# Kernel optimization log

Hardware: AMD Instinct MI355X
Metric: run time of the kernel (lower is better)

## Reference

```python
import jax, jax.numpy as jnp
import numpy as np

TOP_K = 2

def _expert(x, w1, w2, w3):
    return (jax.nn.silu(x @ w1.T) * (x @ w3.T)) @ w2.T

def setup_inputs() -> dict:
    key = jax.random.key(0)
    ks = jax.random.split(key, 8)
    B, L, D, F, E, S = 4, 2048, 1024, 512, 16, 1
    p = lambda k, shape: (jax.random.normal(k, shape, jnp.float32) * 0.02)
    return {
        "x": jax.random.normal(ks[0], (B, L, D), jnp.float32),
        "gate_w": p(ks[1], (E, D)),
        "expert_bias": jnp.zeros((E,), jnp.float32),
        "sw1": p(ks[2], (S, F, D)),
        "sw2": p(ks[3], (S, D, F)),
        "sw3": p(ks[4], (S, F, D)),
        "ew1": p(ks[5], (E, F, D)),
        "ew2": p(ks[6], (E, D, F)),
        "ew3": p(ks[7], (E, F, D)),
    }

def reference(x, gate_w, expert_bias, sw1, sw2, sw3, ew1, ew2, ew3):
    B, L, D = x.shape
    E = gate_w.shape[0]
    flat_x = x.reshape(-1, D)  # [T, D], T = B*L

    # Shared experts (always-on)
    shared = sum(_expert(flat_x, sw1[i], sw2[i], sw3[i]) for i in range(sw1.shape[0]))

    # Router (eval mode: no jitter noise, no bias update; expert_bias buffer added)
    logits = flat_x @ gate_w.T + expert_bias          # [T, E]
    probs = jax.nn.softmax(logits, axis=-1)
    topw, topi = jax.lax.top_k(probs, TOP_K)          # [T, k]
    topw = topw / jnp.sum(topw, axis=-1, keepdims=True)

    # Routed experts: combine weight per (token, expert); zero weight => zero contribution,
    # identical math to the masked gather/scatter in the original.
    out = jnp.zeros_like(flat_x)
    for e in range(E):  # fixed small structural loop over experts
        cw = jnp.sum(jnp.where(topi == e, topw, 0.0), axis=-1)  # [T]
        out = out + cw[:, None] * _expert(flat_x, ew1[e], ew2[e], ew3[e])

    y = (shared + out).reshape(B, L, D)
    return y, probs
```

## Files before the change

### kernel.cpp

```cpp
#include <hip/hip_runtime.h>

typedef unsigned short u16;
typedef __bf16 bf16_t;
typedef bf16_t bf16x8 __attribute__((ext_vector_type(8)));
typedef float f32x4 __attribute__((ext_vector_type(4)));

#define T_TOK 8192
#define DIM   1024
#define FF    512
#define NE    16
#define RBASE_SHARED (2 * T_TOK)
#define NROWS (RBASE_SHARED + T_TOK)
#define MAXTILES 256
#define NSEG 512

__device__ __forceinline__ u16 f2bf(float f) {
  union { float f; unsigned u; } v; v.f = f;
  unsigned r = v.u + 0x7FFFu + ((v.u >> 16) & 1u);
  return (u16)(r >> 16);
}
__device__ __forceinline__ float bf2f(u16 h) {
  union { unsigned u; float f; } v; v.u = ((unsigned)h) << 16; return v.f;
}
__device__ __forceinline__ int clampi(int v, int lo, int hi) {
  return v < lo ? lo : (v > hi ? hi : v);
}

#define GLL16(g, l) __builtin_amdgcn_global_load_lds( \
    (const __attribute__((address_space(1))) void*)(g), \
    (__attribute__((address_space(3))) void*)(l), 16, 0, 0)

#define WAIT_VM_BARRIER(n) asm volatile("s_waitcnt vmcnt(" #n ")\n\ts_barrier" ::: "memory")
#define BARRIER_ONLY()     asm volatile("s_barrier" ::: "memory")
#define WAIT_LGKM0()       asm volatile("s_waitcnt lgkmcnt(0)" ::: "memory")

#define X4   2097152
#define SW4  131072
#define EW4  2097152
#define TOT4 (X4 + 3 * SW4 + 3 * EW4)

__global__ __launch_bounds__(256) void cvt_all_kernel(
    const float* __restrict__ x, const float* __restrict__ sw1,
    const float* __restrict__ sw2, const float* __restrict__ sw3,
    const float* __restrict__ ew1, const float* __restrict__ ew2,
    const float* __restrict__ ew3,
    u16* __restrict__ xb, u16* __restrict__ sw1b, u16* __restrict__ sw2b,
    u16* __restrict__ sw3b, u16* __restrict__ ew1b, u16* __restrict__ ew2b,
    u16* __restrict__ ew3b) {
  int i = blockIdx.x * 256 + threadIdx.x;
  const float* s; u16* dst; int j;
  if (i < X4)                       { s = x;   dst = xb;   j = i; }
  else if (i < X4 + SW4)            { s = sw1; dst = sw1b; j = i - X4; }
  else if (i < X4 + 2 * SW4)        { s = sw2; dst = sw2b; j = i - (X4 + SW4); }
  else if (i < X4 + 3 * SW4)        { s = sw3; dst = sw3b; j = i - (X4 + 2 * SW4); }
  else if (i < X4 + 3 * SW4 + EW4)      { s = ew1; dst = ew1b; j = i - (X4 + 3 * SW4); }
  else if (i < X4 + 3 * SW4 + 2 * EW4)  { s = ew2; dst = ew2b; j = i - (X4 + 3 * SW4 + EW4); }
  else if (i < TOT4)                    { s = ew3; dst = ew3b; j = i - (X4 + 3 * SW4 + 2 * EW4); }
  else return;
  float4 v = reinterpret_cast<const float4*>(s)[j];
  ushort4 o;
  o.x = f2bf(v.x); o.y = f2bf(v.y); o.z = f2bf(v.z); o.w = f2bf(v.w);
  reinterpret_cast<ushort4*>(dst)[j] = o;
}

__global__ __launch_bounds__(256) void router_kernel(
    const float* __restrict__ x, const float* __restrict__ gw,
    const float* __restrict__ ebias, float* __restrict__ probs,
    int* __restrict__ topi, float* __restrict__ topw, int* __restrict__ cnt_seg) {
  __shared__ int hist[16];
  int tid = threadIdx.x;
  int lane = tid & 63, w = tid >> 6;
  if (tid < 16) hist[tid] = 0;
  __syncthreads();
  const float4* gv = reinterpret_cast<const float4*>(gw);
  for (int it = 0; it < 2; ++it) {
    int t0 = blockIdx.x * 16 + (w + 4 * it) * 2;
    const float4* x0 = reinterpret_cast<const float4*>(x + (size_t)t0 * DIM);
    const float4* x1 = reinterpret_cast<const float4*>(x + (size_t)(t0 + 1) * DIM);
    float4 xa[4], xc[4];
#pragma unroll
    for (int j = 0; j < 4; ++j) { xa[j] = x0[j * 64 + lane]; xc[j] = x1[j * 64 + lane]; }
    float p0[16], p1[16];
#pragma unroll
    for (int e = 0; e < NE; ++e) {
      float s0 = 0.f, s1 = 0.f;
#pragma unroll
      for (int j = 0; j < 4; ++j) {
        float4 g = gv[e * 256 + j * 64 + lane];
        s0 += xa[j].x * g.x + xa[j].y * g.y + xa[j].z * g.z + xa[j].w * g.w;
        s1 += xc[j].x * g.x + xc[j].y * g.y + xc[j].z * g.z + xc[j].w * g.w;
      }
#pragma unroll
      for (int d = 1; d < 64; d <<= 1) { s0 += __shfl_xor(s0, d); s1 += __shfl_xor(s1, d); }
      float b = ebias[e];
      p0[e] = s0 + b; p1[e] = s1 + b;
    }
    float m0 = p0[0], m1 = p1[0];
#pragma unroll
    for (int e = 1; e < NE; ++e) { m0 = fmaxf(m0, p0[e]); m1 = fmaxf(m1, p1[e]); }
    float sum0 = 0.f, sum1 = 0.f;
#pragma unroll
    for (int e = 0; e < NE; ++e) {
      p0[e] = __expf(p0[e] - m0); sum0 += p0[e];
      p1[e] = __expf(p1[e] - m1); sum1 += p1[e];
    }
    float inv0 = 1.f / sum0, inv1 = 1.f / sum1;
#pragma unroll
    for (int e = 0; e < NE; ++e) { p0[e] *= inv0; p1[e] *= inv1; }
    if (lane == 0) {
#pragma unroll
      for (int j = 0; j < 4; ++j)
        reinterpret_cast<float4*>(probs + (size_t)t0 * NE)[j] =
            make_float4(p0[4 * j], p0[4 * j + 1], p0[4 * j + 2], p0[4 * j + 3]);
      float b1 = -1.f, b2 = -1.f; int i1 = 0, i2 = 0;
#pragma unroll
      for (int e = 0; e < NE; ++e) {
        float pe = p0[e];
        if (pe > b1) { b2 = b1; i2 = i1; b1 = pe; i1 = e; }
        else if (pe > b2) { b2 = pe; i2 = e; }
      }
      float ws = b1 + b2;
      reinterpret_cast<int2*>(topi)[t0] = make_int2(i1, i2);
      reinterpret_cast<float2*>(topw)[t0] = make_float2(b1 / ws, b2 / ws);
      atomicAdd(&hist[i1], 1); atomicAdd(&hist[i2], 1);
    }
    if (lane == 1) {
      int t1 = t0 + 1;
#pragma unroll
      for (int j = 0; j < 4; ++j)
        reinterpret_cast<float4*>(probs + (size_t)t1 * NE)[j] =
            make_float4(p1[4 * j], p1[4 * j + 1], p1[4 * j + 2], p1[4 * j + 3]);
      float b1 = -1.f, b2 = -1.f; int i1 = 0, i2 = 0;
#pragma unroll
      for (int e = 0; e < NE; ++e) {
        float pe = p1[e];
        if (pe > b1) { b2 = b1; i2 = i1; b1 = pe; i1 = e; }
        else if (pe > b2) { b2 = pe; i2 = e; }
      }
      float ws = b1 + b2;
      reinterpret_cast<int2*>(topi)[t1] = make_int2(i1, i2);
      reinterpret_cast<float2*>(topw)[t1] = make_float2(b1 / ws, b2 / ws);
      atomicAdd(&hist[i1], 1); atomicAdd(&hist[i2], 1);
    }
  }
  __syncthreads();
  if (tid < 16) cnt_seg[blockIdx.x * 16 + tid] = hist[tid];
}

__global__ __launch_bounds__(256) void scan_kernel(
    const int* __restrict__ cnt_seg, int* __restrict__ cnt, int* __restrict__ offs,
    int* __restrict__ seg_base, int2* __restrict__ tab) {
  __shared__ int chunk_sum[16][16];
  __shared__ int chunk_base[16][16];
  __shared__ int tot[16], off_s[17];
  int tid = threadIdx.x;
  int e = tid & 15, c = tid >> 4;
  int s0 = 0;
  for (int s = 0; s < 32; ++s) s0 += cnt_seg[(c * 32 + s) * 16 + e];
  chunk_sum[c][e] = s0;
  __syncthreads();
  if (tid < 16) {
    int r = 0;
    for (int c2 = 0; c2 < 16; ++c2) { chunk_base[c2][tid] = r; r += chunk_sum[c2][tid]; }
    tot[tid] = r;
  }
  __syncthreads();
  if (tid == 0) {
    int a = 0;
    for (int i = 0; i < 16; ++i) { off_s[i] = a; offs[i] = a; cnt[i] = tot[i]; a += tot[i]; }
    off_s[16] = RBASE_SHARED; offs[16] = RBASE_SHARED;
    for (int i = 0; i < MAXTILES; ++i) tab[i] = make_int2(-1, 0);
    int loadc[8]  = {0, 0, 0, 0, 0, 0, 0, 0};
    int cursor[8] = {0, 0, 0, 0, 0, 0, 0, 0};
    for (int g = 0; g < 16; ++g) {
      int nt = (tot[g] + 127) >> 7;
      if (nt == 0) continue;
      int best = 0;
      for (int c2 = 1; c2 < 8; ++c2) if (loadc[c2] < loadc[best]) best = c2;
      loadc[best] += nt;
      int c2 = best;
      for (int ti = 0; ti < nt; ++ti) {
        while (cursor[c2] >= 32) c2 = (c2 + 1) & 7;
        tab[c2 * 32 + cursor[c2]] = make_int2(g, ti * 128);
        cursor[c2]++;
      }
    }
    for (int ti = 0; ti < 64; ++ti) {
      int c2 = ti & 7;
      while (cursor[c2] >= 32) c2 = (c2 + 1) & 7;
      tab[c2 * 32 + cursor[c2]] = make_int2(16, ti * 128);
      cursor[c2]++;
    }
  }
  __syncthreads();
  int r = off_s[e] + chunk_base[c][e];
  for (int s = 0; s < 32; ++s) {
    int seg = c * 32 + s;
    seg_base[seg * 16 + e] = r;
    r += cnt_seg[seg * 16 + e];
  }
}

__global__ __launch_bounds__(64) void scatter_kernel(
    const int* __restrict__ topi, const float* __restrict__ topw,
    const int* __restrict__ seg_base,
    int* __restrict__ idx, float* __restrict__ cwl, int* __restrict__ slotmap) {
  __shared__ int ti[16][2]; __shared__ float tw[16][2]; __shared__ int base[16];
  int b = blockIdx.x;
  int tid = threadIdx.x;
  if (tid < 16) {
    int t = b * 16 + tid;
    int2 pp = reinterpret_cast<const int2*>(topi)[t];
    ti[tid][0] = clampi(pp.x, 0, 15); ti[tid][1] = clampi(pp.y, 0, 15);
    float2 ww = reinterpret_cast<const float2*>(topw)[t];
    tw[tid][0] = ww.x; tw[tid][1] = ww.y;
    base[tid] = seg_base[b * 16 + tid];
  }
  __syncthreads();
  if (tid < 32) {
    int l = tid >> 1, s = tid & 1;
    int t = b * 16 + l;
    int e = ti[l][s];
    int rank = 0;
    for (int t2 = 0; t2 < 16; ++t2) {
      if (ti[t2][0] == e && (t2 < l || (t2 == l && 0 < s))) ++rank;
      if (ti[t2][1] == e && (t2 < l)) ++rank;
    }
    int slot = clampi(base[e] + rank, 0, NROWS - 1);
    idx[slot] = t; cwl[slot] = tw[l][s]; slotmap[t * 3 + s] = slot;
  } else if (tid < 48) {
    int l = tid - 32;
    int t = b * 16 + l;
    int sh = RBASE_SHARED + t;
    idx[sh] = t; cwl[sh] = 1.0f; slotmap[t * 3 + 2] = sh;
  }
}

__global__ __launch_bounds__(256, 2) void gemm_silu_kernel(
    const u16* __restrict__ A, const u16* __restrict__ sw1b, const u16* __restrict__ sw3b,
    const u16* __restrict__ ew1b, const u16* __restrict__ ew3b, u16* __restrict__ G,
    const int2* __restrict__ tab, const int* __restrict__ offs,
    const int* __restrict__ cnt, const int* __restrict__ gidx) {
  const int K = DIM;
  int orig = blockIdx.x;
  int xcd = orig & 7;
  int q = orig >> 3;
  int slot = q & 31, ny = q >> 5;
  int tileid = xcd * 32 + slot;
  int2 te = tab[tileid];
  int e = te.x;
  if (e < 0) return;
  e = clampi(e, 0, NE);
  int m0 = te.y;
  int M = (e == NE) ? T_TOK : cnt[e];
  M = clampi(M, 1, T_TOK);
  int rowbase = clampi(offs[e], 0, NROWS - 1);
  const u16* B1 = (e == NE) ? sw1b : ew1b + (size_t)e * FF * K;
  const u16* B3 = (e == NE) ? sw3b : ew3b + (size_t)e * FF * K;
  int n0 = ny * 128;

  __shared__ u16 As[3 * 4096], B1s[3 * 4096], B3s[3 * 4096];

  int tid = threadIdx.x;
  int lane = tid & 63, wv = tid >> 6;
  int srow = tid >> 2, sg = tid & 3;
  int sk0 = (sg ^ ((srow >> 1) & 3)) * 8;
  int sk1 = (sg ^ (((srow + 64) >> 1) & 3)) * 8;
  int r0 = min(m0 + srow, M - 1);
  int r1 = min(m0 + srow + 64, M - 1);
  int ga0 = clampi(gidx[clampi(rowbase + r0, 0, NROWS - 1)], 0, T_TOK - 1);
  int ga1 = clampi(gidx[clampi(rowbase + r1, 0, NROWS - 1)], 0, T_TOK - 1);
  const u16* Ap0 = A + (size_t)ga0 * K + sk0;
  const u16* Ap1 = A + (size_t)ga1 * K + sk1;
  const u16* B1p0 = B1 + (size_t)(n0 + srow) * K + sk0;
  const u16* B1p1 = B1 + (size_t)(n0 + srow + 64) * K + sk1;
  const u16* B3p0 = B3 + (size_t)(n0 + srow) * K + sk0;
  const u16* B3p1 = B3 + (size_t)(n0 + srow + 64) * K + sk1;
  int st0 = wv * 512, st1 = 2048 + wv * 512;

  int ln15 = lane & 15, qd = lane >> 4;
  int qsw = (qd ^ ((ln15 >> 1) & 3)) * 8;
  int wm = (wv >> 1) * 64, wn = (wv & 1) * 64;
  int aoff = (wm + ln15) * 32 + qsw;
  int boff = (wn + ln15) * 32 + qsw;

  f32x4 acc1[4][4] = {};
  f32x4 acc3[4][4] = {};

#pragma unroll
  for (int b = 0; b < 3; ++b) {
    const int bb = b * 4096, kb = b * 32;
    GLL16(Ap0 + kb, As + bb + st0);      GLL16(Ap1 + kb, As + bb + st1);
    GLL16(B1p0 + kb, B1s + bb + st0);    GLL16(B1p1 + kb, B1s + bb + st1);
    GLL16(B3p0 + kb, B3s + bb + st0);    GLL16(B3p1 + kb, B3s + bb + st1);
  }

#pragma unroll
  for (int t = 0; t < 29; ++t) {
    const int cur = (t % 3) * 4096;
    WAIT_VM_BARRIER(12);
    bf16x8 af[4], bx[4];
#pragma unroll
    for (int i = 0; i < 4; ++i) {
      af[i] = *reinterpret_cast<const bf16x8*>(&As[cur + aoff + i * 512]);
      bx[i] = *reinterpret_cast<const bf16x8*>(&B1s[cur + boff + i * 512]);
    }
    WAIT_LGKM0();
    __builtin_amdgcn_sched_barrier(0);
    __builtin_amdgcn_s_setprio(1);
#pragma unroll
    for (int i = 0; i < 4; ++i)
#pragma unroll
      for (int j = 0; j < 4; ++j)
        acc1[i][j] = __builtin_amdgcn_mfma_f32_16x16x32_bf16(af[i], bx[j], acc1[i][j], 0, 0, 0);
    __builtin_amdgcn_s_setprio(0);
    __builtin_amdgcn_sched_barrier(0);
#pragma unroll
    for (int i = 0; i < 4; ++i)
      bx[i] = *reinterpret_cast<const bf16x8*>(&B3s[cur + boff + i * 512]);
    WAIT_LGKM0();
    __builtin_amdgcn_sched_barrier(0);
    BARRIER_ONLY();
    const int kt = (t + 3) * 32;
    GLL16(Ap0 + kt, As + cur + st0);     GLL16(Ap1 + kt, As + cur + st1);
    GLL16(B1p0 + kt, B1s + cur + st0);   GLL16(B1p1 + kt, B1s + cur + st1);
    GLL16(B3p0 + kt, B3s + cur + st0);   GLL16(B3p1 + kt, B3s + cur + st1);
    __builtin_amdgcn_s_setprio(1);
#pragma unroll
    for (int i = 0; i < 4; ++i)
#pragma unroll
      for (int j = 0; j < 4; ++j)
        acc3[i][j] = __builtin_amdgcn_mfma_f32_16x16x32_bf16(af[i], bx[j], acc3[i][j], 0, 0, 0);
    __builtin_amdgcn_s_setprio(0);
  }
#pragma unroll
  for (int pt = 29; pt < 32; ++pt) {
    const int cur = (pt % 3) * 4096;
    if (pt == 29)      { WAIT_VM_BARRIER(12); }
    else if (pt == 30) { WAIT_VM_BARRIER(6); }
    else               { WAIT_VM_BARRIER(0); }
    bf16x8 af[4], bx[4];
#pragma unroll
    for (int i = 0; i < 4; ++i) {
      af[i] = *reinterpret_cast<const bf16x8*>(&As[cur + aoff + i * 512]);
      bx[i] = *reinterpret_cast<const bf16x8*>(&B1s[cur + boff + i * 512]);
    }
    WAIT_LGKM0();
    __builtin_amdgcn_sched_barrier(0);
    __builtin_amdgcn_s_setprio(1);
#pragma unroll
    for (int i = 0; i < 4; ++i)
#pragma unroll
      for (int j = 0; j < 4; ++j)
        acc1[i][j] = __builtin_amdgcn_mfma_f32_16x16x32_bf16(af[i], bx[j], acc1[i][j], 0, 0, 0);
    __builtin_amdgcn_s_setprio(0);
    __builtin_amdgcn_sched_barrier(0);
#pragma unroll
    for (int i = 0; i < 4; ++i)
      bx[i] = *reinterpret_cast<const bf16x8*>(&B3s[cur + boff + i * 512]);
    WAIT_LGKM0();
    __builtin_amdgcn_sched_barrier(0);
    __builtin_amdgcn_s_setprio(1);
#pragma unroll
    for (int i = 0; i < 4; ++i)
#pragma unroll
      for (int j = 0; j < 4; ++j)
        acc3[i][j] = __builtin_amdgcn_mfma_f32_16x16x32_bf16(af[i], bx[j], acc3[i][j], 0, 0, 0);
    __builtin_amdgcn_s_setprio(0);
  }

  int mrem = M - m0;
#pragma unroll
  for (int i = 0; i < 4; ++i)
#pragma unroll
    for (int r2 = 0; r2 < 4; ++r2) {
      int ml = wm + i * 16 + qd * 4 + r2;
      if (ml < mrem) {
        size_t orow = (size_t)clampi(rowbase + m0 + ml, 0, NROWS - 1);
#pragma unroll
        for (int j = 0; j < 4; ++j) {
          float z1 = acc1[i][j][r2], z3 = acc3[i][j][r2];
          float g = z1 / (1.f + __expf(-z1)) * z3;
          G[orow * FF + n0 + wn + j * 16 + ln15] = f2bf(g);
        }
      }
    }
}

__global__ __launch_bounds__(256, 2) void gemm_out_kernel(
    const u16* __restrict__ Gb, const u16* __restrict__ sw2b, const u16* __restrict__ ew2b,
    u16* __restrict__ O, const int2* __restrict__ tab, const int* __restrict__ offs,
    const int* __restrict__ cnt, const float* __restrict__ cwl) {
  const int K = FF;
  int orig = blockIdx.x;
  int xcd = orig & 7;
  int q = orig >> 3;
  int slot = q & 31, ny = q >> 5;
  int tileid = xcd * 32 + slot;
  int2 te = tab[tileid];
  int e = te.x;
  if (e < 0) return;
  e = clampi(e, 0, NE);
  int m0 = te.y;
  int M = (e == NE) ? T_TOK : cnt[e];
  M = clampi(M, 1, T_TOK);
  int rowbase = clampi(offs[e], 0, NROWS - 1);
  const u16* B = (e == NE) ? sw2b : ew2b + (size_t)e * DIM * K;
  int n0 = ny * 128;

  __shared__ u16 As[3 * 4096], Bs[3 * 4096];

  int tid = threadIdx.x;
  int lane = tid & 63, wv = tid >> 6;
  int srow = tid >> 2, sg = tid & 3;
  int sk0 = (sg ^ ((srow >> 1) & 3)) * 8;
  int sk1 = (sg ^ (((srow + 64) >> 1) & 3)) * 8;
  int r0 = clampi(rowbase + min(m0 + srow, M - 1), 0, NROWS - 1);
  int r1 = clampi(rowbase + min(m0 + srow + 64, M - 1), 0, NROWS - 1);
  const u16* Ap0 = Gb + (size_t)r0 * K + sk0;
  const u16* Ap1 = Gb + (size_t)r1 * K + sk1;
  const u16* Bp0 = B + (size_t)(n0 + srow) * K + sk0;
  const u16* Bp1 = B + (size_t)(n0 + srow + 64) * K + sk1;
  int st0 = wv * 512, st1 = 2048 + wv * 512;

  int ln15 = lane & 15, qd = lane >> 4;
  int qsw = (qd ^ ((ln15 >> 1) & 3)) * 8;
  int wm = (wv >> 1) * 64, wn = (wv & 1) * 64;
  int aoff = (wm + ln15) * 32 + qsw;
  int boff = (wn + ln15) * 32 + qsw;

  f32x4 acc[4][4] = {};

#pragma unroll
  for (int b = 0; b < 3; ++b) {
    const int bb = b * 4096, kb = b * 32;
    GLL16(Ap0 + kb, As + bb + st0);   GLL16(Ap1 + kb, As + bb + st1);
    GLL16(Bp0 + kb, Bs + bb + st0);   GLL16(Bp1 + kb, Bs + bb + st1);
  }

#pragma unroll
  for (int t = 0; t < 13; ++t) {
    const int cur = (t % 3) * 4096;
    WAIT_VM_BARRIER(8);
    bf16x8 af[4], bf[4];
#pragma unroll
    for (int i = 0; i < 4; ++i) {
      af[i] = *reinterpret_cast<const bf16x8*>(&As[cur + aoff + i * 512]);
      bf[i] = *reinterpret_cast<const bf16x8*>(&Bs[cur + boff + i * 512]);
    }
    WAIT_LGKM0();
    __builtin_amdgcn_sched_barrier(0);
    BARRIER_ONLY();
    const int kt = (t + 3) * 32;
    GLL16(Ap0 + kt, As + cur + st0);   GLL16(Ap1 + kt, As + cur + st1);
    GLL16(Bp0 + kt, Bs + cur + st0);   GLL16(Bp1 + kt, Bs + cur + st1);
    __builtin_amdgcn_s_setprio(1);
#pragma unroll
    for (int i = 0; i < 4; ++i)
#pragma unroll
      for (int j = 0; j < 4; ++j)
        acc[i][j] = __builtin_amdgcn_mfma_f32_16x16x32_bf16(af[i], bf[j], acc[i][j], 0, 0, 0);
    __builtin_amdgcn_s_setprio(0);
  }
#pragma unroll
  for (int pt = 13; pt < 16; ++pt) {
    const int cur = (pt % 3) * 4096;
    if (pt == 13)      { WAIT_VM_BARRIER(8); }
    else if (pt == 14) { WAIT_VM_BARRIER(4); }
    else               { WAIT_VM_BARRIER(0); }
    bf16x8 af[4], bf[4];
#pragma unroll
    for (int i = 0; i < 4; ++i) {
      af[i] = *reinterpret_cast<const bf16x8*>(&As[cur + aoff + i * 512]);
      bf[i] = *reinterpret_cast<const bf16x8*>(&Bs[cur + boff + i * 512]);
    }
    WAIT_LGKM0();
    __builtin_amdgcn_sched_barrier(0);
    __builtin_amdgcn_s_setprio(1);
#pragma unroll
    for (int i = 0; i < 4; ++i)
#pragma unroll
      for (int j = 0; j < 4; ++j)
        acc[i][j] = __builtin_amdgcn_mfma_f32_16x16x32_bf16(af[i], bf[j], acc[i][j], 0, 0, 0);
    __builtin_amdgcn_s_setprio(0);
  }

  int mrem = M - m0;
#pragma unroll
  for (int i = 0; i < 4; ++i)
#pragma unroll
    for (int r2 = 0; r2 < 4; ++r2) {
      int ml = wm + i * 16 + qd * 4 + r2;
      if (ml < mrem) {
        int slot2 = clampi(rowbase + m0 + ml, 0, NROWS - 1);
        float cw = cwl[slot2];
#pragma unroll
        for (int j = 0; j < 4; ++j)
          O[(size_t)slot2 * DIM + n0 + wn + j * 16 + ln15] = f2bf(acc[i][j][r2] * cw);
      }
    }
}

__global__ __launch_bounds__(256) void combine_kernel(
    const u16* __restrict__ O, const int* __restrict__ slotmap, float* __restrict__ y) {
  int t = blockIdx.x;
  int c = threadIdx.x;
  int s0 = clampi(slotmap[t * 3], 0, NROWS - 1);
  int s1 = clampi(slotmap[t * 3 + 1], 0, NROWS - 1);
  int s2 = clampi(slotmap[t * 3 + 2], 0, NROWS - 1);
  ushort4 a = reinterpret_cast<const ushort4*>(O + (size_t)s0 * DIM)[c];
  ushort4 b = reinterpret_cast<const ushort4*>(O + (size_t)s1 * DIM)[c];
  ushort4 d = reinterpret_cast<const ushort4*>(O + (size_t)s2 * DIM)[c];
  float4 r;
  r.x = bf2f(a.x) + bf2f(b.x) + bf2f(d.x);
  r.y = bf2f(a.y) + bf2f(b.y) + bf2f(d.y);
  r.z = bf2f(a.z) + bf2f(b.z) + bf2f(d.z);
  r.w = bf2f(a.w) + bf2f(b.w) + bf2f(d.w);
  reinterpret_cast<float4*>(y + (size_t)t * DIM)[c] = r;
}

extern "C" void kernel_launch(void* const* d_in, const int* in_sizes, int n_in,
                              void* d_out, int out_size, void* d_ws, size_t ws_size,
                              hipStream_t stream) {
  const float* x     = (const float*)d_in[0];
  const float* gw    = (const float*)d_in[1];
  const float* ebias = (const float*)d_in[2];
  const float* sw1   = (const float*)d_in[3];
  const float* sw2   = (const float*)d_in[4];
  const float* sw3   = (const float*)d_in[5];
  const float* ew1   = (const float*)d_in[6];
  const float* ew2   = (const float*)d_in[7];
  const float* ew3   = (const float*)d_in[8];
  float* y = (float*)d_out;
  float* probs = y + (size_t)T_TOK * DIM;

  char* ws = (char*)d_ws;
  size_t o = 0;
  auto alloc = [&](size_t bytes) -> char* {
    char* p = ws + o;
    o = (o + bytes + 255) & ~(size_t)255;
    return p;
  };
  u16* G    = (u16*)alloc((size_t)NROWS * FF * 2);
  u16* sw1b = (u16*)alloc((size_t)FF * DIM * 2);
  u16* sw2b = (u16*)alloc((size_t)FF * DIM * 2);
  u16* sw3b = (u16*)alloc((size_t)FF * DIM * 2);
  u16* ew2b = (u16*)alloc((size_t)NE * FF * DIM * 2);
  char* aliasBase = alloc((size_t)NROWS * DIM * 2);
  u16* xb   = (u16*)aliasBase;
  u16* ew1b = (u16*)(aliasBase + (size_t)T_TOK * DIM * 2);
  u16* ew3b = (u16*)(aliasBase + (size_t)T_TOK * DIM * 2 + (size_t)NE * FF * DIM * 2);
  u16* O    = (u16*)aliasBase;
  int*   topi    = (int*)alloc(T_TOK * 2 * 4);
  float* topw    = (float*)alloc(T_TOK * 2 * 4);
  int*   idx     = (int*)alloc(NROWS * 4);
  float* cwl     = (float*)alloc(NROWS * 4);
  int*   slotmap = (int*)alloc(T_TOK * 3 * 4);
  int2*  tab     = (int2*)alloc(MAXTILES * 8);
  int*   cnt_seg = (int*)alloc(NSEG * 16 * 4);
  int*   seg_base= (int*)alloc(NSEG * 16 * 4);
  int*   cnt     = (int*)alloc(256);
  int*   offs    = (int*)alloc(256);

  router_kernel<<<NSEG, 256, 0, stream>>>(x, gw, ebias, probs, topi, topw, cnt_seg);
  scan_kernel<<<1, 256, 0, stream>>>(cnt_seg, cnt, offs, seg_base, tab);
  scatter_kernel<<<NSEG, 64, 0, stream>>>(topi, topw, seg_base, idx, cwl, slotmap);
  cvt_all_kernel<<<TOT4 / 256, 256, 0, stream>>>(x, sw1, sw2, sw3, ew1, ew2, ew3,
                                                 xb, sw1b, sw2b, sw3b, ew1b, ew2b, ew3b);

  gemm_silu_kernel<<<1024, 256, 0, stream>>>(
      xb, sw1b, sw3b, ew1b, ew3b, G, tab, offs, cnt, idx);
  gemm_out_kernel<<<2048, 256, 0, stream>>>(
      G, sw2b, ew2b, O, tab, offs, cnt, cwl);
  combine_kernel<<<T_TOK, 256, 0, stream>>>(O, slotmap, y);
}
```

Measured before the change: 389.7 us.

## Fuse x bf16 conversion into router; drop per-step second barrier in GEMM pipelines

The router kernel now writes the bf16 copy of x from the fp32 values it has already loaded, so the convert kernel only handles weights and x is not read a second time. Both GEMM kernels change their triple-buffered LDS pipeline from prefetch depth 3 with two barriers per k-step to prefetch depth 2. The next tile is issued into the free buffer right after the single wait+barrier, which removes one s_barrier per iteration. In exchange there is less load latency slack, and the router does more stores, which could lengthen that kernel.

```diff
diff --git a/kernel.cpp b/kernel.cpp
--- a/kernel.cpp
+++ b/kernel.cpp
@@ -31,31 +31,26 @@
     (__attribute__((address_space(3))) void*)(l), 16, 0, 0)
 
 #define WAIT_VM_BARRIER(n) asm volatile("s_waitcnt vmcnt(" #n ")\n\ts_barrier" ::: "memory")
-#define BARRIER_ONLY()     asm volatile("s_barrier" ::: "memory")
 #define WAIT_LGKM0()       asm volatile("s_waitcnt lgkmcnt(0)" ::: "memory")
 
-#define X4   2097152
 #define SW4  131072
 #define EW4  2097152
-#define TOT4 (X4 + 3 * SW4 + 3 * EW4)
+#define TOTW4 (3 * SW4 + 3 * EW4)
 
 __global__ __launch_bounds__(256) void cvt_all_kernel(
-    const float* __restrict__ x, const float* __restrict__ sw1,
-    const float* __restrict__ sw2, const float* __restrict__ sw3,
-    const float* __restrict__ ew1, const float* __restrict__ ew2,
-    const float* __restrict__ ew3,
-    u16* __restrict__ xb, u16* __restrict__ sw1b, u16* __restrict__ sw2b,
-    u16* __restrict__ sw3b, u16* __restrict__ ew1b, u16* __restrict__ ew2b,
-    u16* __restrict__ ew3b) {
+    const float* __restrict__ sw1, const float* __restrict__ sw2,
+    const float* __restrict__ sw3, const float* __restrict__ ew1,
+    const float* __restrict__ ew2, const float* __restrict__ ew3,
+    u16* __restrict__ sw1b, u16* __restrict__ sw2b, u16* __restrict__ sw3b,
+    u16* __restrict__ ew1b, u16* __restrict__ ew2b, u16* __restrict__ ew3b) {
   int i = blockIdx.x * 256 + threadIdx.x;
   const float* s; u16* dst; int j;
-  if (i < X4)                       { s = x;   dst = xb;   j = i; }
-  else if (i < X4 + SW4)            { s = sw1; dst = sw1b; j = i - X4; }
-  else if (i < X4 + 2 * SW4)        { s = sw2; dst = sw2b; j = i - (X4 + SW4); }
-  else if (i < X4 + 3 * SW4)        { s = sw3; dst = sw3b; j = i - (X4 + 2 * SW4); }
-  else if (i < X4 + 3 * SW4 + EW4)      { s = ew1; dst = ew1b; j = i - (X4 + 3 * SW4); }
-  else if (i < X4 + 3 * SW4 + 2 * EW4)  { s = ew2; dst = ew2b; j = i - (X4 + 3 * SW4 + EW4); }
-  else if (i < TOT4)                    { s = ew3; dst = ew3b; j = i - (X4 + 3 * SW4 + 2 * EW4); }
+  if (i < SW4)                      { s = sw1; dst = sw1b; j = i; }
+  else if (i < 2 * SW4)             { s = sw2; dst = sw2b; j = i - SW4; }
+  else if (i < 3 * SW4)             { s = sw3; dst = sw3b; j = i - 2 * SW4; }
+  else if (i < 3 * SW4 + EW4)       { s = ew1; dst = ew1b; j = i - 3 * SW4; }
+  else if (i < 3 * SW4 + 2 * EW4)   { s = ew2; dst = ew2b; j = i - (3 * SW4 + EW4); }
+  else if (i < TOTW4)               { s = ew3; dst = ew3b; j = i - (3 * SW4 + 2 * EW4); }
   else return;
   float4 v = reinterpret_cast<const float4*>(s)[j];
   ushort4 o;
@@ -66,7 +61,8 @@
 __global__ __launch_bounds__(256) void router_kernel(
     const float* __restrict__ x, const float* __restrict__ gw,
     const float* __restrict__ ebias, float* __restrict__ probs,
-    int* __restrict__ topi, float* __restrict__ topw, int* __restrict__ cnt_seg) {
+    int* __restrict__ topi, float* __restrict__ topw, int* __restrict__ cnt_seg,
+    u16* __restrict__ xb) {
   __shared__ int hist[16];
   int tid = threadIdx.x;
   int lane = tid & 63, w = tid >> 6;
@@ -80,6 +76,16 @@
     float4 xa[4], xc[4];
 #pragma unroll
     for (int j = 0; j < 4; ++j) { xa[j] = x0[j * 64 + lane]; xc[j] = x1[j * 64 + lane]; }
+    u16* xr0 = xb + (size_t)t0 * DIM;
+    u16* xr1 = xb + (size_t)(t0 + 1) * DIM;
+#pragma unroll
+    for (int j = 0; j < 4; ++j) {
+      ushort4 o0, o1;
+      o0.x = f2bf(xa[j].x); o0.y = f2bf(xa[j].y); o0.z = f2bf(xa[j].z); o0.w = f2bf(xa[j].w);
+      o1.x = f2bf(xc[j].x); o1.y = f2bf(xc[j].y); o1.z = f2bf(xc[j].z); o1.w = f2bf(xc[j].w);
+      reinterpret_cast<ushort4*>(xr0)[j * 64 + lane] = o0;
+      reinterpret_cast<ushort4*>(xr1)[j * 64 + lane] = o1;
+    }
     float p0[16], p1[16];
 #pragma unroll
     for (int e = 0; e < NE; ++e) {
@@ -288,7 +294,7 @@
   f32x4 acc3[4][4] = {};
 
 #pragma unroll
-  for (int b = 0; b < 3; ++b) {
+  for (int b = 0; b < 2; ++b) {
     const int bb = b * 4096, kb = b * 32;
     GLL16(Ap0 + kb, As + bb + st0);      GLL16(Ap1 + kb, As + bb + st1);
     GLL16(B1p0 + kb, B1s + bb + st0);    GLL16(B1p1 + kb, B1s + bb + st1);
@@ -296,9 +302,14 @@
   }
 
 #pragma unroll
-  for (int t = 0; t < 29; ++t) {
+  for (int t = 0; t < 30; ++t) {
     const int cur = (t % 3) * 4096;
-    WAIT_VM_BARRIER(12);
+    WAIT_VM_BARRIER(6);
+    const int nxt = ((t + 2) % 3) * 4096;
+    const int kt = (t + 2) * 32;
+    GLL16(Ap0 + kt, As + nxt + st0);     GLL16(Ap1 + kt, As + nxt + st1);
+    GLL16(B1p0 + kt, B1s + nxt + st0);   GLL16(B1p1 + kt, B1s + nxt + st1);
+    GLL16(B3p0 + kt, B3s + nxt + st0);   GLL16(B3p1 + kt, B3s + nxt + st1);
     bf16x8 af[4], bx[4];
 #pragma unroll
     for (int i = 0; i < 4; ++i) {
@@ -320,11 +331,6 @@
       bx[i] = *reinterpret_cast<const bf16x8*>(&B3s[cur + boff + i * 512]);
     WAIT_LGKM0();
     __builtin_amdgcn_sched_barrier(0);
-    BARRIER_ONLY();
-    const int kt = (t + 3) * 32;
-    GLL16(Ap0 + kt, As + cur + st0);     GLL16(Ap1 + kt, As + cur + st1);
-    GLL16(B1p0 + kt, B1s + cur + st0);   GLL16(B1p1 + kt, B1s + cur + st1);
-    GLL16(B3p0 + kt, B3s + cur + st0);   GLL16(B3p1 + kt, B3s + cur + st1);
     __builtin_amdgcn_s_setprio(1);
 #pragma unroll
     for (int i = 0; i < 4; ++i)
@@ -334,11 +340,10 @@
     __builtin_amdgcn_s_setprio(0);
   }
 #pragma unroll
-  for (int pt = 29; pt < 32; ++pt) {
+  for (int pt = 30; pt < 32; ++pt) {
     const int cur = (pt % 3) * 4096;
-    if (pt == 29)      { WAIT_VM_BARRIER(12); }
-    else if (pt == 30) { WAIT_VM_BARRIER(6); }
-    else               { WAIT_VM_BARRIER(0); }
+    if (pt == 30) { WAIT_VM_BARRIER(6); }
+    else          { WAIT_VM_BARRIER(0); }
     bf16x8 af[4], bx[4];
 #pragma unroll
     for (int i = 0; i < 4; ++i) {
@@ -432,16 +437,20 @@
   f32x4 acc[4][4] = {};
 
 #pragma unroll
-  for (int b = 0; b < 3; ++b) {
+  for (int b = 0; b < 2; ++b) {
     const int bb = b * 4096, kb = b * 32;
     GLL16(Ap0 + kb, As + bb + st0);   GLL16(Ap1 + kb, As + bb + st1);
     GLL16(Bp0 + kb, Bs + bb + st0);   GLL16(Bp1 + kb, Bs + bb + st1);
   }
 
 #pragma unroll
-  for (int t = 0; t < 13; ++t) {
+  for (int t = 0; t < 14; ++t) {
     const int cur = (t % 3) * 4096;
-    WAIT_VM_BARRIER(8);
+    WAIT_VM_BARRIER(4);
+    const int nxt = ((t + 2) % 3) * 4096;
+    const int kt = (t + 2) * 32;
+    GLL16(Ap0 + kt, As + nxt + st0);   GLL16(Ap1 + kt, As + nxt + st1);
+    GLL16(Bp0 + kt, Bs + nxt + st0);   GLL16(Bp1 + kt, Bs + nxt + st1);
     bf16x8 af[4], bf[4];
 #pragma unroll
     for (int i = 0; i < 4; ++i) {
@@ -450,10 +459,6 @@
     }
     WAIT_LGKM0();
     __builtin_amdgcn_sched_barrier(0);
-    BARRIER_ONLY();
-    const int kt = (t + 3) * 32;
-    GLL16(Ap0 + kt, As + cur + st0);   GLL16(Ap1 + kt, As + cur + st1);
-    GLL16(Bp0 + kt, Bs + cur + st0);   GLL16(Bp1 + kt, Bs + cur + st1);
     __builtin_amdgcn_s_setprio(1);
 #pragma unroll
     for (int i = 0; i < 4; ++i)
@@ -463,11 +468,10 @@
     __builtin_amdgcn_s_setprio(0);
   }
 #pragma unroll
-  for (int pt = 13; pt < 16; ++pt) {
+  for (int pt = 14; pt < 16; ++pt) {
     const int cur = (pt % 3) * 4096;
-    if (pt == 13)      { WAIT_VM_BARRIER(8); }
-    else if (pt == 14) { WAIT_VM_BARRIER(4); }
-    else               { WAIT_VM_BARRIER(0); }
+    if (pt == 14) { WAIT_VM_BARRIER(4); }
+    else          { WAIT_VM_BARRIER(0); }
     bf16x8 af[4], bf[4];
 #pragma unroll
     for (int i = 0; i < 4; ++i) {
@@ -562,11 +566,11 @@
   int*   cnt     = (int*)alloc(256);
   int*   offs    = (int*)alloc(256);
 
-  router_kernel<<<NSEG, 256, 0, stream>>>(x, gw, ebias, probs, topi, topw, cnt_seg);
+  router_kernel<<<NSEG, 256, 0, stream>>>(x, gw, ebias, probs, topi, topw, cnt_seg, xb);
   scan_kernel<<<1, 256, 0, stream>>>(cnt_seg, cnt, offs, seg_base, tab);
   scatter_kernel<<<NSEG, 64, 0, stream>>>(topi, topw, seg_base, idx, cwl, slotmap);
-  cvt_all_kernel<<<TOT4 / 256, 256, 0, stream>>>(x, sw1, sw2, sw3, ew1, ew2, ew3,
-                                                 xb, sw1b, sw2b, sw3b, ew1b, ew2b, ew3b);
+  cvt_all_kernel<<<TOTW4 / 256, 256, 0, stream>>>(sw1, sw2, sw3, ew1, ew2, ew3,
+                                                  sw1b, sw2b, sw3b, ew1b, ew2b, ew3b);
 
   gemm_silu_kernel<<<1024, 256, 0, stream>>>(
       xb, sw1b, sw3b, ew1b, ew3b, G, tab, offs, cnt, idx);
```

After: 380.8 us. 2.3% less time.
